# Kernel optimization log

Hardware: AMD Instinct MI355X
Metric: run time of the kernel (lower is better)

## Reference

```python
import jax, jax.numpy as jnp
import numpy as np

N_NODES = 100000
N_EDGES = 1600000
IN_CH = 128
HID = 128
N_GNN = 3
OUT_CH = 2
EPS = 1e-12  # F.normalize clamp


def setup_inputs() -> dict:
    key = jax.random.key(0)
    ks = jax.random.split(key, 8)
    s = 0.05
    return {
        "x": jax.random.normal(ks[0], (N_NODES, IN_CH), jnp.float32),
        "edge_index": jax.random.randint(ks[1], (2, N_EDGES), 0, N_NODES, jnp.int32),
        "Wl": jax.random.normal(ks[2], (N_GNN, HID, IN_CH), jnp.float32) * s,
        "bl": jnp.zeros((N_GNN, HID), jnp.float32),
        "Wr": jax.random.normal(ks[3], (N_GNN, HID, IN_CH), jnp.float32) * s,
        "Wlin1": jax.random.normal(ks[4], (HID, HID), jnp.float32) * s,
        "blin1": jnp.zeros((HID,), jnp.float32),
        "Wlin2": jax.random.normal(ks[5], (OUT_CH, HID), jnp.float32) * s,
        "blin2": jnp.zeros((OUT_CH,), jnp.float32),
    }


def reference(x, edge_index, Wl, bl, Wr, Wlin1, blin1, Wlin2, blin2):
    src, dst = edge_index[0], edge_index[1]
    n = x.shape[0]
    # in-degree for mean aggregation (zero-degree nodes -> divide by 1)
    deg = jax.ops.segment_sum(jnp.ones_like(src, x.dtype), dst, num_segments=n)
    inv_deg = (1.0 / jnp.maximum(deg, 1.0))[:, None]  # [N,1]
    for i in range(Wl.shape[0]):
        mean_nb = jax.ops.segment_sum(x[src], dst, num_segments=n) * inv_deg  # [N,H]
        out = mean_nb @ Wl[i].T + bl[i] + x @ Wr[i].T  # SAGEConv
        # normalize=True -> L2 normalize rows
        out = out / jnp.maximum(jnp.linalg.norm(out, axis=-1, keepdims=True), EPS)
        x = jax.nn.relu(out)  # dropout is identity in eval
    x = jax.nn.relu(x @ Wlin1.T + blin1)
    return x @ Wlin2.T + blin2
```

## Files before the change

kernel.cpp:

```cpp
#include <hip/hip_runtime.h>

#define N_NODES 100000
#define N_EDGES 1600000
#define HID 128
#define N_GNN 3
#define OUT_CH 2
#define EPS 1e-12f

#define SCAN_BLOCK 256
#define SCAN_ITEMS 8
#define SCAN_CHUNK 2048
#define SCAN_NBLOCKS ((N_NODES + SCAN_CHUNK - 1) / SCAN_CHUNK)

typedef __attribute__((ext_vector_type(8))) short short8;
typedef __attribute__((ext_vector_type(4))) float f32x4;

__global__ void k_deg(const int* __restrict__ dst, int* __restrict__ deg, int E) {
    int i = blockIdx.x * blockDim.x + threadIdx.x;
    if (i < E) atomicAdd(&deg[dst[i]], 1);
}

__global__ __launch_bounds__(SCAN_BLOCK) void k_scan_block(const int* __restrict__ deg,
                                                           int* __restrict__ offs,
                                                           int* __restrict__ bsum) {
    __shared__ int ts[SCAN_BLOCK];
    const int base = blockIdx.x * SCAN_CHUNK + threadIdx.x * SCAN_ITEMS;
    int v[SCAN_ITEMS];
    int s = 0;
#pragma unroll
    for (int k = 0; k < SCAN_ITEMS; ++k) {
        int idx = base + k;
        v[k] = (idx < N_NODES) ? deg[idx] : 0;
        s += v[k];
    }
    ts[threadIdx.x] = s;
    __syncthreads();
    for (int d = 1; d < SCAN_BLOCK; d <<= 1) {
        int t = (threadIdx.x >= d) ? ts[threadIdx.x - d] : 0;
        __syncthreads();
        ts[threadIdx.x] += t;
        __syncthreads();
    }
    int run = ts[threadIdx.x] - s;
#pragma unroll
    for (int k = 0; k < SCAN_ITEMS; ++k) {
        int idx = base + k;
        if (idx < N_NODES) offs[idx] = run;
        run += v[k];
    }
    if (threadIdx.x == SCAN_BLOCK - 1) bsum[blockIdx.x] = ts[SCAN_BLOCK - 1];
}

__global__ void k_scan_sums(int* __restrict__ bsum, int nb) {
    if (blockIdx.x == 0 && threadIdx.x == 0) {
        int run = 0;
        for (int i = 0; i < nb; ++i) { int v = bsum[i]; bsum[i] = run; run += v; }
    }
}

__global__ void k_finalize(const int* __restrict__ deg, int* __restrict__ offs,
                           const int* __restrict__ bsum, int* __restrict__ cursor,
                           float* __restrict__ ideg, int n) {
    int i = blockIdx.x * 256 + threadIdx.x;
    if (i >= n) return;
    int o = offs[i] + bsum[i >> 11];
    offs[i] = o;
    cursor[i] = o;
    ideg[i] = 1.0f / fmaxf((float)deg[i], 1.0f);
}

__global__ void k_bucket(const int* __restrict__ ei, int* __restrict__ cursor,
                         int* __restrict__ nbr, int E) {
    int e = blockIdx.x * 256 + threadIdx.x;
    if (e >= E) return;
    int dst = ei[N_EDGES + e];
    int pos = atomicAdd(&cursor[dst], 1);
    nbr[pos] = ei[e];
}

__global__ __launch_bounds__(256) void k_gather(const float* __restrict__ x,
                                                const int* __restrict__ offs,
                                                const int* __restrict__ deg,
                                                const float* __restrict__ ideg,
                                                const int* __restrict__ nbr,
                                                float* __restrict__ agg, int n) {
    int node = blockIdx.x * 8 + (threadIdx.x >> 5);
    if (node >= n) return;
    int lane = threadIdx.x & 31;
    int off = offs[node], d = deg[node];
    f32x4 a = {0.f, 0.f, 0.f, 0.f};
    int j = 0;
    for (; j + 8 <= d; j += 8) {
        int s[8];
#pragma unroll
        for (int u = 0; u < 8; ++u) s[u] = nbr[off + j + u];
#pragma unroll
        for (int u = 0; u < 8; ++u)
            a += *reinterpret_cast<const f32x4*>(x + (size_t)s[u] * HID + lane * 4);
    }
    for (; j < d; ++j) {
        int s = nbr[off + j];
        a += *reinterpret_cast<const f32x4*>(x + (size_t)s * HID + lane * 4);
    }
    f32x4 o = a * ideg[node];
    *reinterpret_cast<f32x4*>(agg + (size_t)node * HID + lane * 4) = o;
}

__global__ void k_makefrags(const float* __restrict__ Wl, const float* __restrict__ Wr,
                            const float* __restrict__ Wlin1,
                            unsigned short* __restrict__ fhi,
                            unsigned short* __restrict__ flo) {
    int t = blockIdx.x * 256 + threadIdx.x;
    if (t >= 7 * 16384) return;
    int j  = t & 7;
    int l  = (t >> 3) & 63;
    int ks = (t >> 9) & 3;
    int nt = (t >> 11) & 7;
    int m  = t >> 14;
    int c = nt * 16 + (l & 15);
    int k = ks * 32 + ((l >> 4) & 3) * 8 + j;
    const float* src = (m < 3) ? (Wl + m * 16384)
                     : (m < 6) ? (Wr + (m - 3) * 16384)
                               : Wlin1;
    float a = src[c * 128 + k];
    unsigned u  = __float_as_uint(a);
    unsigned uh = u & 0xffff0000u;
    float r = a - __uint_as_float(uh);
    fhi[t] = (unsigned short)(uh >> 16);
    flo[t] = (unsigned short)(__float_as_uint(r) >> 16);
}

__device__ __forceinline__ void split8(const f32x4 a0, const f32x4 a1,
                                       short8& h, short8& l) {
    float a[8] = {a0[0], a0[1], a0[2], a0[3], a1[0], a1[1], a1[2], a1[3]};
#pragma unroll
    for (int j = 0; j < 8; ++j) {
        unsigned u  = __float_as_uint(a[j]);
        unsigned uh = u & 0xffff0000u;
        h[j] = (short)(uh >> 16);
        float r = a[j] - __uint_as_float(uh);
        l[j] = (short)(__float_as_uint(r) >> 16);
    }
}

__global__ __launch_bounds__(256) void k_sage_mfma(
    const float* __restrict__ xin, const float* __restrict__ agg,
    const unsigned short* __restrict__ fhi, const unsigned short* __restrict__ flo,
    int lmat, const float* __restrict__ bl, float* __restrict__ xout, int n) {
    const int l  = threadIdx.x & 63;
    const int lr = l & 15, lk = l >> 4;
    const int row0 = blockIdx.x * 64 + (threadIdx.x >> 6) * 16;
    const int gr = row0 + lr;
    const bool rok = gr < n;

    f32x4 acc[8];
#pragma unroll
    for (int nt = 0; nt < 8; ++nt) {
        float b = bl[nt * 16 + lr];
        f32x4 t = {b, b, b, b};
        acc[nt] = t;
    }

    const size_t abase = (size_t)gr * HID + lk * 8;
#pragma unroll
    for (int ks = 0; ks < 4; ++ks) {
        f32x4 a0 = {0.f,0.f,0.f,0.f}, a1 = a0, x0 = a0, x1 = a0;
        if (rok) {
            const f32x4* ap = reinterpret_cast<const f32x4*>(agg + abase + ks * 32);
            const f32x4* xp = reinterpret_cast<const f32x4*>(xin + abase + ks * 32);
            a0 = ap[0]; a1 = ap[1];
            x0 = xp[0]; x1 = xp[1];
        }
        short8 ah, al, xh, xl;
        split8(a0, a1, ah, al);
        split8(x0, x1, xh, xl);

        const int foL = ((lmat * 8) * 4 + ks) * 512 + l * 8;
        const int foR = (((3 + lmat) * 8) * 4 + ks) * 512 + l * 8;
#pragma unroll
        for (int nt = 0; nt < 8; ++nt) {
            short8 blh = *reinterpret_cast<const short8*>(fhi + foL + nt * 2048);
            short8 bll = *reinterpret_cast<const short8*>(flo + foL + nt * 2048);
            short8 brh = *reinterpret_cast<const short8*>(fhi + foR + nt * 2048);
            short8 brl = *reinterpret_cast<const short8*>(flo + foR + nt * 2048);
            acc[nt] = __builtin_amdgcn_mfma_f32_16x16x32_bf16(ah, blh, acc[nt], 0, 0, 0);
            acc[nt] = __builtin_amdgcn_mfma_f32_16x16x32_bf16(al, blh, acc[nt], 0, 0, 0);
            acc[nt] = __builtin_amdgcn_mfma_f32_16x16x32_bf16(ah, bll, acc[nt], 0, 0, 0);
            acc[nt] = __builtin_amdgcn_mfma_f32_16x16x32_bf16(xh, brh, acc[nt], 0, 0, 0);
            acc[nt] = __builtin_amdgcn_mfma_f32_16x16x32_bf16(xl, brh, acc[nt], 0, 0, 0);
            acc[nt] = __builtin_amdgcn_mfma_f32_16x16x32_bf16(xh, brl, acc[nt], 0, 0, 0);
        }
    }

#pragma unroll
    for (int i = 0; i < 4; ++i) {
        float v[8];
        float ss = 0.f;
#pragma unroll
        for (int nt = 0; nt < 8; ++nt) { v[nt] = acc[nt][i]; ss += v[nt] * v[nt]; }
#pragma unroll
        for (int m = 1; m < 16; m <<= 1) ss += __shfl_xor(ss, m, 64);
        float inv = 1.0f / fmaxf(sqrtf(ss), EPS);
        int orow = row0 + lk * 4 + i;
        if (orow < n) {
#pragma unroll
            for (int nt = 0; nt < 8; ++nt)
                xout[(size_t)orow * HID + nt * 16 + lr] = fmaxf(v[nt] * inv, 0.f);
        }
    }
}

__global__ __launch_bounds__(256) void k_final_mfma(
    const float* __restrict__ xin,
    const unsigned short* __restrict__ fhi, const unsigned short* __restrict__ flo,
    const float* __restrict__ b1, const float* __restrict__ W2,
    const float* __restrict__ b2, float* __restrict__ out, int n) {
    const int l  = threadIdx.x & 63;
    const int lr = l & 15, lk = l >> 4;
    const int row0 = blockIdx.x * 64 + (threadIdx.x >> 6) * 16;
    const int gr = row0 + lr;
    const bool rok = gr < n;

    f32x4 acc[8];
#pragma unroll
    for (int nt = 0; nt < 8; ++nt) {
        float b = b1[nt * 16 + lr];
        f32x4 t = {b, b, b, b};
        acc[nt] = t;
    }

    const size_t abase = (size_t)gr * HID + lk * 8;
#pragma unroll
    for (int ks = 0; ks < 4; ++ks) {
        f32x4 x0 = {0.f,0.f,0.f,0.f}, x1 = x0;
        if (rok) {
            const f32x4* xp = reinterpret_cast<const f32x4*>(xin + abase + ks * 32);
            x0 = xp[0]; x1 = xp[1];
        }
        short8 xh, xl;
        split8(x0, x1, xh, xl);
        const int fo = ((6 * 8) * 4 + ks) * 512 + l * 8;
#pragma unroll
        for (int nt = 0; nt < 8; ++nt) {
            short8 bh = *reinterpret_cast<const short8*>(fhi + fo + nt * 2048);
            short8 blo = *reinterpret_cast<const short8*>(flo + fo + nt * 2048);
            acc[nt] = __builtin_amdgcn_mfma_f32_16x16x32_bf16(xh, bh, acc[nt], 0, 0, 0);
            acc[nt] = __builtin_amdgcn_mfma_f32_16x16x32_bf16(xl, bh, acc[nt], 0, 0, 0);
            acc[nt] = __builtin_amdgcn_mfma_f32_16x16x32_bf16(xh, blo, acc[nt], 0, 0, 0);
        }
    }

    float w20[8], w21[8];
#pragma unroll
    for (int nt = 0; nt < 8; ++nt) {
        w20[nt] = W2[nt * 16 + lr];
        w21[nt] = W2[HID + nt * 16 + lr];
    }
#pragma unroll
    for (int i = 0; i < 4; ++i) {
        float p0 = 0.f, p1 = 0.f;
#pragma unroll
        for (int nt = 0; nt < 8; ++nt) {
            float h = fmaxf(acc[nt][i], 0.f);
            p0 += h * w20[nt];
            p1 += h * w21[nt];
        }
#pragma unroll
        for (int m = 1; m < 16; m <<= 1) {
            p0 += __shfl_xor(p0, m, 64);
            p1 += __shfl_xor(p1, m, 64);
        }
        int orow = row0 + lk * 4 + i;
        if (lr == 0 && orow < n) {
            out[(size_t)orow * 2 + 0] = p0 + b2[0];
            out[(size_t)orow * 2 + 1] = p1 + b2[1];
        }
    }
}

extern "C" void kernel_launch(void* const* d_in, const int* in_sizes, int n_in,
                              void* d_out, int out_size, void* d_ws, size_t ws_size,
                              hipStream_t stream) {
    const float* x     = (const float*)d_in[0];
    const int*   ei    = (const int*)  d_in[1];
    const float* Wl    = (const float*)d_in[2];
    const float* bl    = (const float*)d_in[3];
    const float* Wr    = (const float*)d_in[4];
    const float* Wlin1 = (const float*)d_in[5];
    const float* blin1 = (const float*)d_in[6];
    const float* Wlin2 = (const float*)d_in[7];
    const float* blin2 = (const float*)d_in[8];
    float* out = (float*)d_out;

    float* xbuf = (float*)d_ws;
    float* agg  = xbuf + (size_t)N_NODES * HID;
    float* ideg = agg  + (size_t)N_NODES * HID;
    unsigned short* fhi = (unsigned short*)(ideg + N_NODES);
    unsigned short* flo = fhi + 7 * 16384;
    int* deg    = (int*)(flo + 7 * 16384);
    int* offs   = deg + N_NODES;
    int* cursor = offs + N_NODES;
    int* bsum   = cursor + N_NODES;
    int* nbr    = bsum + 64;

    hipMemsetAsync(deg, 0, N_NODES * sizeof(int), stream);
    k_deg<<<(N_EDGES + 255) / 256, 256, 0, stream>>>(ei + N_EDGES, deg, N_EDGES);
    k_scan_block<<<SCAN_NBLOCKS, SCAN_BLOCK, 0, stream>>>(deg, offs, bsum);
    k_scan_sums<<<1, 64, 0, stream>>>(bsum, SCAN_NBLOCKS);
    k_finalize<<<(N_NODES + 255) / 256, 256, 0, stream>>>(deg, offs, bsum, cursor,
                                                          ideg, N_NODES);
    k_bucket<<<(N_EDGES + 255) / 256, 256, 0, stream>>>(ei, cursor, nbr, N_EDGES);
    k_makefrags<<<(7 * 16384 + 255) / 256, 256, 0, stream>>>(Wl, Wr, Wlin1, fhi, flo);

    const int mm_grid = (N_NODES + 63) / 64;
    const int gather_grid = (N_NODES + 7) / 8;
    for (int l = 0; l < N_GNN; ++l) {
        const float* xin = (l == 0) ? x : xbuf;
        k_gather<<<gather_grid, 256, 0, stream>>>(xin, offs, deg, ideg, nbr, agg,
                                                  N_NODES);
        k_sage_mfma<<<mm_grid, 256, 0, stream>>>(xin, agg, fhi, flo, l,
                                                 bl + (size_t)l * HID, xbuf, N_NODES);
    }
    k_final_mfma<<<mm_grid, 256, 0, stream>>>(xbuf, fhi, flo, blin1, Wlin2, blin2,
                                              out, N_NODES);
}
```

Baseline: 849.4 us.

## Build CSR via two-level bucket partition with shared-memory histograms

Replaces the global-atomic degree count, three-kernel scan and per-edge global atomic bucketing with a two-pass partition. Edges are first binned into buckets of 256 destination nodes using shared-memory histograms, then each bucket is sorted locally into CSR order in shared memory. This is meant to cut contended global atomics and scattered writes during graph preprocessing. It adds an extra packed edge buffer and a serial single-thread scan over about 391 buckets, and it relies on source ids fitting in 24 bits.

```diff
diff --git a/kernel.cpp b/kernel.cpp
--- a/kernel.cpp
+++ b/kernel.cpp
@@ -7,75 +7,107 @@
 #define OUT_CH 2
 #define EPS 1e-12f
 
-#define SCAN_BLOCK 256
-#define SCAN_ITEMS 8
-#define SCAN_CHUNK 2048
-#define SCAN_NBLOCKS ((N_NODES + SCAN_CHUNK - 1) / SCAN_CHUNK)
+#define NPB 256
+#define NBUCK ((N_NODES + NPB - 1) / NPB)
+#define EPB 4096
+#define EBLOCKS ((N_EDGES + EPB - 1) / EPB)
 
 typedef __attribute__((ext_vector_type(8))) short short8;
 typedef __attribute__((ext_vector_type(4))) float f32x4;
 
-__global__ void k_deg(const int* __restrict__ dst, int* __restrict__ deg, int E) {
-    int i = blockIdx.x * blockDim.x + threadIdx.x;
-    if (i < E) atomicAdd(&deg[dst[i]], 1);
-}
-
-__global__ __launch_bounds__(SCAN_BLOCK) void k_scan_block(const int* __restrict__ deg,
-                                                           int* __restrict__ offs,
-                                                           int* __restrict__ bsum) {
-    __shared__ int ts[SCAN_BLOCK];
-    const int base = blockIdx.x * SCAN_CHUNK + threadIdx.x * SCAN_ITEMS;
-    int v[SCAN_ITEMS];
-    int s = 0;
-#pragma unroll
-    for (int k = 0; k < SCAN_ITEMS; ++k) {
-        int idx = base + k;
-        v[k] = (idx < N_NODES) ? deg[idx] : 0;
-        s += v[k];
-    }
-    ts[threadIdx.x] = s;
-    __syncthreads();
-    for (int d = 1; d < SCAN_BLOCK; d <<= 1) {
-        int t = (threadIdx.x >= d) ? ts[threadIdx.x - d] : 0;
-        __syncthreads();
-        ts[threadIdx.x] += t;
-        __syncthreads();
-    }
-    int run = ts[threadIdx.x] - s;
-#pragma unroll
-    for (int k = 0; k < SCAN_ITEMS; ++k) {
-        int idx = base + k;
-        if (idx < N_NODES) offs[idx] = run;
-        run += v[k];
-    }
-    if (threadIdx.x == SCAN_BLOCK - 1) bsum[blockIdx.x] = ts[SCAN_BLOCK - 1];
-}
-
-__global__ void k_scan_sums(int* __restrict__ bsum, int nb) {
+__global__ __launch_bounds__(256) void k_hist(const int* __restrict__ dst,
+                                              int* __restrict__ bcnt, int E) {
+    __shared__ int h[NBUCK];
+    for (int i = threadIdx.x; i < NBUCK; i += 256) h[i] = 0;
+    __syncthreads();
+    int e0 = blockIdx.x * EPB;
+    int e1 = e0 + EPB < E ? e0 + EPB : E;
+    for (int e = e0 + threadIdx.x; e < e1; e += 256)
+        atomicAdd(&h[dst[e] >> 8], 1);
+    __syncthreads();
+    for (int i = threadIdx.x; i < NBUCK; i += 256) {
+        int v = h[i];
+        if (v) atomicAdd(&bcnt[i], v);
+    }
+}
+
+__global__ void k_bscan(const int* __restrict__ bcnt, int* __restrict__ boffs,
+                        int* __restrict__ gcur) {
     if (blockIdx.x == 0 && threadIdx.x == 0) {
         int run = 0;
-        for (int i = 0; i < nb; ++i) { int v = bsum[i]; bsum[i] = run; run += v; }
-    }
-}
-
-__global__ void k_finalize(const int* __restrict__ deg, int* __restrict__ offs,
-                           const int* __restrict__ bsum, int* __restrict__ cursor,
-                           float* __restrict__ ideg, int n) {
-    int i = blockIdx.x * 256 + threadIdx.x;
-    if (i >= n) return;
-    int o = offs[i] + bsum[i >> 11];
-    offs[i] = o;
-    cursor[i] = o;
-    ideg[i] = 1.0f / fmaxf((float)deg[i], 1.0f);
-}
-
-__global__ void k_bucket(const int* __restrict__ ei, int* __restrict__ cursor,
-                         int* __restrict__ nbr, int E) {
-    int e = blockIdx.x * 256 + threadIdx.x;
-    if (e >= E) return;
-    int dst = ei[N_EDGES + e];
-    int pos = atomicAdd(&cursor[dst], 1);
-    nbr[pos] = ei[e];
+        for (int i = 0; i < NBUCK; ++i) {
+            boffs[i] = run;
+            gcur[i] = run;
+            run += bcnt[i];
+        }
+        boffs[NBUCK] = run;
+    }
+}
+
+__global__ __launch_bounds__(256) void k_part(const int* __restrict__ ei,
+                                              int* __restrict__ gcur,
+                                              unsigned* __restrict__ part, int E) {
+    __shared__ int h[NBUCK], base[NBUCK];
+    for (int i = threadIdx.x; i < NBUCK; i += 256) h[i] = 0;
+    __syncthreads();
+    int e0 = blockIdx.x * EPB;
+    int e1 = e0 + EPB < E ? e0 + EPB : E;
+    for (int e = e0 + threadIdx.x; e < e1; e += 256)
+        atomicAdd(&h[ei[N_EDGES + e] >> 8], 1);
+    __syncthreads();
+    for (int i = threadIdx.x; i < NBUCK; i += 256) {
+        int v = h[i];
+        base[i] = v ? atomicAdd(&gcur[i], v) : 0;
+        h[i] = 0;
+    }
+    __syncthreads();
+    for (int e = e0 + threadIdx.x; e < e1; e += 256) {
+        int d = ei[N_EDGES + e], s = ei[e];
+        int b = d >> 8;
+        int p = base[b] + atomicAdd(&h[b], 1);
+        part[p] = ((unsigned)(d & 255) << 24) | (unsigned)s;
+    }
+}
+
+__global__ __launch_bounds__(256) void k_csr(const unsigned* __restrict__ part,
+                                             const int* __restrict__ boffs,
+                                             int* __restrict__ deg,
+                                             int* __restrict__ offs,
+                                             float* __restrict__ ideg,
+                                             int* __restrict__ nbr, int n) {
+    __shared__ int d[NPB], sc[NPB], cur[NPB];
+    const int tid = threadIdx.x;
+    const int node0 = blockIdx.x << 8;
+    const int p0 = boffs[blockIdx.x], p1 = boffs[blockIdx.x + 1];
+    d[tid] = 0;
+    __syncthreads();
+    for (int p = p0 + tid; p < p1; p += 256)
+        atomicAdd(&d[part[p] >> 24], 1);
+    __syncthreads();
+    int v = d[tid];
+    sc[tid] = v;
+    __syncthreads();
+    for (int o = 1; o < NPB; o <<= 1) {
+        int t = (tid >= o) ? sc[tid - o] : 0;
+        __syncthreads();
+        sc[tid] += t;
+        __syncthreads();
+    }
+    int excl = sc[tid] - v;
+    int node = node0 + tid;
+    if (node < n) {
+        offs[node] = p0 + excl;
+        deg[node] = v;
+        ideg[node] = 1.0f / fmaxf((float)v, 1.0f);
+    }
+    cur[tid] = excl;
+    __syncthreads();
+    for (int p = p0 + tid; p < p1; p += 256) {
+        unsigned u = part[p];
+        int dl = u >> 24;
+        int pos = p0 + atomicAdd(&cur[dl], 1);
+        nbr[pos] = (int)(u & 0xFFFFFFu);
+    }
 }
 
 __global__ __launch_bounds__(256) void k_gather(const float* __restrict__ x,
@@ -299,17 +331,17 @@
     unsigned short* flo = fhi + 7 * 16384;
     int* deg    = (int*)(flo + 7 * 16384);
     int* offs   = deg + N_NODES;
-    int* cursor = offs + N_NODES;
-    int* bsum   = cursor + N_NODES;
-    int* nbr    = bsum + 64;
-
-    hipMemsetAsync(deg, 0, N_NODES * sizeof(int), stream);
-    k_deg<<<(N_EDGES + 255) / 256, 256, 0, stream>>>(ei + N_EDGES, deg, N_EDGES);
-    k_scan_block<<<SCAN_NBLOCKS, SCAN_BLOCK, 0, stream>>>(deg, offs, bsum);
-    k_scan_sums<<<1, 64, 0, stream>>>(bsum, SCAN_NBLOCKS);
-    k_finalize<<<(N_NODES + 255) / 256, 256, 0, stream>>>(deg, offs, bsum, cursor,
-                                                          ideg, N_NODES);
-    k_bucket<<<(N_EDGES + 255) / 256, 256, 0, stream>>>(ei, cursor, nbr, N_EDGES);
+    int* bcnt   = offs + N_NODES;
+    int* boffs  = bcnt + NBUCK;
+    int* gcur   = boffs + NBUCK + 1;
+    int* nbr    = gcur + NBUCK;
+    unsigned* part = (unsigned*)(nbr + N_EDGES);
+
+    hipMemsetAsync(bcnt, 0, NBUCK * sizeof(int), stream);
+    k_hist<<<EBLOCKS, 256, 0, stream>>>(ei + N_EDGES, bcnt, N_EDGES);
+    k_bscan<<<1, 1, 0, stream>>>(bcnt, boffs, gcur);
+    k_part<<<EBLOCKS, 256, 0, stream>>>(ei, gcur, part, N_EDGES);
+    k_csr<<<NBUCK, 256, 0, stream>>>(part, boffs, deg, offs, ideg, nbr, N_NODES);
     k_makefrags<<<(7 * 16384 + 255) / 256, 256, 0, stream>>>(Wl, Wr, Wlin1, fhi, flo);
 
     const int mm_grid = (N_NODES + 63) / 64;
```

Measured after the change: 719.6 us. -15.3%, faster.
